# Kernel tuning notes

Hardware: AMD Instinct MI355X
Metric: run time of the kernel (lower is better)

Reference implementation:

```python
import jax, jax.numpy as jnp
import numpy as np

B, N, M = 4, 2048, 2048
QUERY_DIM = 512
CONTEXT_DIM = 512
HEADS = 8
DIM_HEAD = 64
INNER = HEADS * DIM_HEAD  # 512
SCALE = DIM_HEAD ** -0.5


def setup_inputs() -> dict:
    key = jax.random.key(0)
    ks = jax.random.split(key, 7)
    x = jax.random.normal(ks[0], (B, N, QUERY_DIM), dtype=jnp.float32)
    context = jax.random.normal(ks[1], (B, M, CONTEXT_DIM), dtype=jnp.float32)
    mask = jax.random.randint(ks[2], (B, M), 0, 2) > 0  # bool key mask
    # Kaiming-uniform-ish init scale, like nn.Linear defaults
    Wq = jax.random.uniform(ks[3], (QUERY_DIM, INNER), dtype=jnp.float32,
                            minval=-1, maxval=1) * (QUERY_DIM ** -0.5)
    Wkv = jax.random.uniform(ks[4], (CONTEXT_DIM, 2 * INNER), dtype=jnp.float32,
                             minval=-1, maxval=1) * (CONTEXT_DIM ** -0.5)
    Wo = jax.random.uniform(ks[5], (INNER, QUERY_DIM), dtype=jnp.float32,
                            minval=-1, maxval=1) * (INNER ** -0.5)
    bo = jax.random.uniform(ks[6], (QUERY_DIM,), dtype=jnp.float32,
                            minval=-1, maxval=1) * (INNER ** -0.5)
    return {"x": x, "context": context, "mask": mask,
            "Wq": Wq, "Wkv": Wkv, "Wo": Wo, "bo": bo}


def reference(x, context, mask, Wq, Wkv, Wo, bo):
    # projections (no bias for q/kv, bias for out — as in the torch module)
    q = x @ Wq                       # [b, n, inner]
    kv = context @ Wkv               # [b, m, 2*inner]
    k, v = jnp.split(kv, 2, axis=-1)
    # split heads: b n (h d) -> b h n d
    def split_heads(t):
        b, n, _ = t.shape
        return t.reshape(b, n, HEADS, DIM_HEAD).transpose(0, 2, 1, 3)
    q, k, v = split_heads(q), split_heads(k), split_heads(v)
    sim = jnp.einsum('bhid,bhjd->bhij', q, k) * SCALE  # [b, h, n, m]
    max_neg = -jnp.finfo(sim.dtype).max
    sim = jnp.where(mask[:, None, None, :], sim, max_neg)
    attn = jax.nn.softmax(sim, axis=-1)
    out = jnp.einsum('bhij,bhjd->bhid', attn, v)       # [b, h, n, d]
    out = out.transpose(0, 2, 1, 3).reshape(x.shape[0], x.shape[1], INNER)
    return out @ Wo + bo
```

## Files before the change

### kernel.cpp

```cpp
#include <hip/hip_runtime.h>
#include <hip/hip_bf16.h>
#include <cstddef>

typedef __attribute__((ext_vector_type(8))) short short8;
typedef __attribute__((ext_vector_type(4))) float f32x4;

__device__ inline unsigned short f2bf(float f) {
  unsigned int u = __float_as_uint(f);
  u += 0x7fffu + ((u >> 16) & 1u);
  return (unsigned short)(u >> 16);
}
__device__ inline unsigned int pkbf(float a, float b) {
  __hip_bfloat162 h = __float22bfloat162_rn(make_float2(a, b));
  union { __hip_bfloat162 h2; unsigned int u; } cv;
  cv.h2 = h;
  return cv.u;
}
__device__ inline float bf2f_lo(unsigned int u) {
  return __uint_as_float(u << 16);
}
__device__ inline float bf2f_hi(unsigned int u) {
  return __uint_as_float(u & 0xFFFF0000u);
}

__global__ __launch_bounds__(256) void prep_kernel(
    const float* __restrict__ Wq, const float* __restrict__ Wkv,
    const float* __restrict__ Wo, const int* __restrict__ mask,
    unsigned short* __restrict__ Wq_t, unsigned short* __restrict__ Wkv_t,
    unsigned short* __restrict__ Wo_t, unsigned int* __restrict__ pmask) {
  const int z = blockIdx.z;
  if (z == 3) {
    if (blockIdx.y != 0) return;
    int idx = blockIdx.x * 256 + threadIdx.x;
    int bb = idx >> 10, rem = idx & 1023;
    int g = rem >> 5, rem2 = rem & 31;
    int lqv = rem2 >> 3, e = rem2 & 7;
    int ct = e >> 1, half = e & 1;
    int key0 = g * 64 + half * 32 + lqv * 8 + 2 * ct;
    const int* mb = mask + bb * 2048;
    pmask[idx] = (mb[key0] ? 0xFFFFu : 0u) | (mb[key0 + 1] ? 0xFFFF0000u : 0u);
    return;
  }
  const float* src = (z == 0) ? Wq : (z == 1) ? Wkv : Wo;
  unsigned short* dst = (z == 0) ? Wq_t : (z == 1) ? Wkv_t : Wo_t;
  const int R = 512, C = (z == 1) ? 1024 : 512;
  if (blockIdx.x * 64 >= C) return;
  __shared__ float tile[64][65];
  int c0 = blockIdx.x * 64, r0 = blockIdx.y * 64;
  int tx = threadIdx.x & 63, ty = threadIdx.x >> 6;
  for (int i = ty; i < 64; i += 4)
    tile[i][tx] = src[(size_t)(r0 + i) * C + c0 + tx];
  __syncthreads();
  for (int i = ty; i < 64; i += 4)
    dst[(size_t)(c0 + i) * R + r0 + tx] = f2bf(tile[tx][i]);
}

__global__ __launch_bounds__(256) void proj_kernel(
    const float* __restrict__ x, const float* __restrict__ context,
    const unsigned short* __restrict__ Wq_t, const unsigned short* __restrict__ Wkv_t,
    unsigned short* __restrict__ qb, unsigned short* __restrict__ kb,
    unsigned short* __restrict__ vtb, float qscale) {
  __shared__ unsigned short As[128][72];
  __shared__ unsigned short Bs[128][72];
  const int bid = blockIdx.x;
  const bool isq = bid < 256;
  const int lid = isq ? bid : bid - 256;
  const float* Af = isq ? x : context;
  const unsigned short* Bt = isq ? Wq_t : Wkv_t;
  const int bn = (isq ? (lid & 3) : (lid & 7)) * 128;
  const int bm = (isq ? (lid >> 2) : (lid >> 3)) * 128;
  const int K = 512;
  const int tid = threadIdx.x;
  const int wave = tid >> 6, lane = tid & 63;
  const int wr = (wave >> 1) * 64, wc = (wave & 1) * 64;
  const int l15 = lane & 15, lq = lane >> 4;
  const int sr = tid >> 3, sc = (tid & 7) * 8;
  f32x4 acc[4][4] = {};

  for (int k0 = 0; k0 < K; k0 += 64) {
    __syncthreads();
#pragma unroll
    for (int p = 0; p < 4; ++p) {
      int r = sr + p * 32;
      const float4 f0 = *(const float4*)(Af + (size_t)(bm + r) * K + k0 + sc);
      const float4 f1 = *(const float4*)(Af + (size_t)(bm + r) * K + k0 + sc + 4);
      uint4 u;
      u.x = pkbf(f0.x, f0.y);
      u.y = pkbf(f0.z, f0.w);
      u.z = pkbf(f1.x, f1.y);
      u.w = pkbf(f1.z, f1.w);
      *(uint4*)(&As[r][sc]) = u;
      *(uint4*)(&Bs[r][sc]) = *(const uint4*)(Bt + (size_t)(bn + r) * K + k0 + sc);
    }
    __syncthreads();
#pragma unroll
    for (int kk = 0; kk < 2; ++kk) {
      short8 af[4], bfr[4];
#pragma unroll
      for (int mt = 0; mt < 4; ++mt)
        af[mt] = *(const short8*)(&As[wr + mt * 16 + l15][kk * 32 + lq * 8]);
#pragma unroll
      for (int nt = 0; nt < 4; ++nt)
        bfr[nt] = *(const short8*)(&Bs[wc + nt * 16 + l15][kk * 32 + lq * 8]);
#pragma unroll
      for (int mt = 0; mt < 4; ++mt)
#pragma unroll
        for (int nt = 0; nt < 4; ++nt)
          acc[mt][nt] = __builtin_amdgcn_mfma_f32_16x16x32_bf16(af[mt], bfr[nt], acc[mt][nt], 0, 0, 0);
    }
  }

#pragma unroll
  for (int mt = 0; mt < 4; ++mt)
#pragma unroll
    for (int nt = 0; nt < 4; ++nt) {
      int row0 = bm + wr + mt * 16 + lq * 4;
      int col = bn + wc + nt * 16 + l15;
      if (isq) {
#pragma unroll
        for (int j = 0; j < 4; ++j)
          qb[(size_t)(row0 + j) * 512 + col] = f2bf(acc[mt][nt][j] * qscale);
      } else if (col < 512) {
#pragma unroll
        for (int j = 0; j < 4; ++j)
          kb[(size_t)(row0 + j) * 512 + col] = f2bf(acc[mt][nt][j]);
      } else {
        int bb = row0 >> 11, m = row0 & 2047;
        int hd = col - 512;
        uint2 w;
        w.x = pkbf(acc[mt][nt][0], acc[mt][nt][1]);
        w.y = pkbf(acc[mt][nt][2], acc[mt][nt][3]);
        *(uint2*)(vtb + ((size_t)bb * 512 + hd) * 2048 + m) = w;
      }
    }
}

__global__ __launch_bounds__(256) void outproj_kernel(
    const unsigned short* __restrict__ poA, const unsigned short* __restrict__ poB,
    const float* __restrict__ ls, const unsigned short* __restrict__ Bt,
    float* __restrict__ C0, const float* __restrict__ bias) {
  __shared__ unsigned short As[64][72];
  __shared__ unsigned short Bs[128][72];
  const int bm = blockIdx.y * 64, bn = blockIdx.x * 128;
  const int K = 512, N = 512;
  const int tid = threadIdx.x;
  const int wave = tid >> 6, lane = tid & 63;
  const int wr = (wave >> 1) * 32, wc = (wave & 1) * 64;
  const int l15 = lane & 15, lq = lane >> 4;
  const int sr = tid >> 3, sc = (tid & 7) * 8;
  f32x4 acc[2][4] = {};

  for (int k0 = 0; k0 < K; k0 += 64) {
    const int h = k0 >> 6;
    __syncthreads();
#pragma unroll
    for (int p = 0; p < 2; ++p) {
      int row = bm + sr + p * 32;
      uint4 ua = *(const uint4*)(poA + (size_t)row * 512 + k0 + sc);
      uint4 ub = *(const uint4*)(poB + (size_t)row * 512 + k0 + sc);
      float l = ls[(size_t)h * 8192 + row] + ls[65536 + (size_t)h * 8192 + row];
      float rl = 1.0f / l;
      uint4 u;
      u.x = pkbf((bf2f_lo(ua.x) + bf2f_lo(ub.x)) * rl, (bf2f_hi(ua.x) + bf2f_hi(ub.x)) * rl);
      u.y = pkbf((bf2f_lo(ua.y) + bf2f_lo(ub.y)) * rl, (bf2f_hi(ua.y) + bf2f_hi(ub.y)) * rl);
      u.z = pkbf((bf2f_lo(ua.z) + bf2f_lo(ub.z)) * rl, (bf2f_hi(ua.z) + bf2f_hi(ub.z)) * rl);
      u.w = pkbf((bf2f_lo(ua.w) + bf2f_lo(ub.w)) * rl, (bf2f_hi(ua.w) + bf2f_hi(ub.w)) * rl);
      *(uint4*)(&As[sr + p * 32][sc]) = u;
    }
#pragma unroll
    for (int p = 0; p < 4; ++p)
      *(uint4*)(&Bs[sr + p * 32][sc]) = *(const uint4*)(Bt + (size_t)(bn + sr + p * 32) * K + k0 + sc);
    __syncthreads();
#pragma unroll
    for (int kk = 0; kk < 2; ++kk) {
      short8 af[2], bfr[4];
#pragma unroll
      for (int mt = 0; mt < 2; ++mt)
        af[mt] = *(const short8*)(&As[wr + mt * 16 + l15][kk * 32 + lq * 8]);
#pragma unroll
      for (int nt = 0; nt < 4; ++nt)
        bfr[nt] = *(const short8*)(&Bs[wc + nt * 16 + l15][kk * 32 + lq * 8]);
#pragma unroll
      for (int mt = 0; mt < 2; ++mt)
#pragma unroll
        for (int nt = 0; nt < 4; ++nt)
          acc[mt][nt] = __builtin_amdgcn_mfma_f32_16x16x32_bf16(af[mt], bfr[nt], acc[mt][nt], 0, 0, 0);
    }
  }

#pragma unroll
  for (int mt = 0; mt < 2; ++mt)
#pragma unroll
    for (int nt = 0; nt < 4; ++nt) {
      int row0 = bm + wr + mt * 16 + lq * 4;
      int col = bn + wc + nt * 16 + l15;
#pragma unroll
      for (int j = 0; j < 4; ++j)
        C0[(size_t)(row0 + j) * N + col] = acc[mt][nt][j] + bias[col];
    }
}

__global__ __launch_bounds__(256, 3) void attn_kernel(
    const unsigned short* __restrict__ Q, const unsigned short* __restrict__ Kb,
    const unsigned short* __restrict__ Vt, const unsigned int* __restrict__ pmask,
    unsigned short* __restrict__ poA, unsigned short* __restrict__ poB,
    float* __restrict__ ls) {
  __shared__ unsigned short Ks[2][64][72];
  __shared__ unsigned short Vs[2][64][72];
  const int b = blockIdx.x >> 3, h = blockIdx.x & 7;
  const int z = blockIdx.z;
  const int tid = threadIdx.x, lane = tid & 63;
  const int wave = tid >> 6;
  const int l15 = lane & 15, lq = lane >> 4;
  const int wrow = blockIdx.y * 128 + wave * 32;

  const unsigned short* Qr0 = Q + (size_t)(b * 2048 + wrow + l15) * 512 + h * 64;
  const unsigned short* Qr1 = Q + (size_t)(b * 2048 + wrow + 16 + l15) * 512 + h * 64;
  short8 q00 = *(const short8*)(Qr0 + lq * 8);
  short8 q01 = *(const short8*)(Qr0 + 32 + lq * 8);
  short8 q10 = *(const short8*)(Qr1 + lq * 8);
  short8 q11 = *(const short8*)(Qr1 + 32 + lq * 8);

  const short8 vones = {0x3F80, 0x3F80, 0x3F80, 0x3F80,
                        0x3F80, 0x3F80, 0x3F80, 0x3F80};

  f32x4 o0[4] = {}, o1[4] = {};
  f32x4 ol0 = {}, ol1 = {};

  const unsigned short* Kg = Kb + (size_t)b * 2048 * 512 + h * 64;
  const unsigned short* Vg = Vt + (size_t)(b * 8 + h) * 64 * 2048;
  const unsigned int* Pm = pmask + b * 1024;

  const int str = tid >> 3;
  const int stc = (tid & 7) * 8;
  const int kprow = ((str & 7) >> 1) * 16 + ((str >> 3) & 3) * 4 + (str & 1);

  const int mb0 = z << 10;

  uint4 krA0 = *(const uint4*)(Kg + (size_t)(mb0 + str) * 512 + stc);
  uint4 krA1 = *(const uint4*)(Kg + (size_t)(mb0 + str + 32) * 512 + stc);
  uint4 krB0 = *(const uint4*)(Kg + (size_t)(mb0 + 64 + str) * 512 + stc);
  uint4 krB1 = *(const uint4*)(Kg + (size_t)(mb0 + 64 + str + 32) * 512 + stc);
  uint4 vrA0 = *(const uint4*)(Vg + (size_t)str * 2048 + mb0 + stc);
  uint4 vrA1 = *(const uint4*)(Vg + (size_t)(str + 32) * 2048 + mb0 + stc);
  uint4 vrB0 = *(const uint4*)(Vg + (size_t)str * 2048 + mb0 + 64 + stc);
  uint4 vrB1 = *(const uint4*)(Vg + (size_t)(str + 32) * 2048 + mb0 + 64 + stc);

  for (int mb = mb0; mb < mb0 + 1024; mb += 128) {
    __syncthreads();
    *(uint4*)(&Ks[0][kprow][stc])     = krA0;
    *(uint4*)(&Ks[0][kprow + 2][stc]) = krA1;
    *(uint4*)(&Ks[1][kprow][stc])     = krB0;
    *(uint4*)(&Ks[1][kprow + 2][stc]) = krB1;
    *(uint4*)(&Vs[0][str][stc])       = vrA0;
    *(uint4*)(&Vs[0][str + 32][stc])  = vrA1;
    *(uint4*)(&Vs[1][str][stc])       = vrB0;
    *(uint4*)(&Vs[1][str + 32][stc])  = vrB1;
    __syncthreads();
    if (mb + 128 < mb0 + 1024) {
      const int nx = mb + 128;
      krA0 = *(const uint4*)(Kg + (size_t)(nx + str) * 512 + stc);
      krA1 = *(const uint4*)(Kg + (size_t)(nx + str + 32) * 512 + stc);
      krB0 = *(const uint4*)(Kg + (size_t)(nx + 64 + str) * 512 + stc);
      krB1 = *(const uint4*)(Kg + (size_t)(nx + 64 + str + 32) * 512 + stc);
      vrA0 = *(const uint4*)(Vg + (size_t)str * 2048 + nx + stc);
      vrA1 = *(const uint4*)(Vg + (size_t)(str + 32) * 2048 + nx + stc);
      vrB0 = *(const uint4*)(Vg + (size_t)str * 2048 + nx + 64 + stc);
      vrB1 = *(const uint4*)(Vg + (size_t)(str + 32) * 2048 + nx + 64 + stc);
    }

#pragma unroll
    for (int g = 0; g < 2; ++g) {
      const uint4 m0 = *(const uint4*)(Pm + ((mb >> 6) + g) * 32 + lq * 8);
      const uint4 m1 = *(const uint4*)(Pm + ((mb >> 6) + g) * 32 + lq * 8 + 4);

      f32x4 s0[4] = {}, s1[4] = {};
#pragma unroll
      for (int ct = 0; ct < 4; ++ct) {
        short8 kf = *(const short8*)(&Ks[g][ct * 16 + l15][lq * 8]);
        s0[ct] = __builtin_amdgcn_mfma_f32_16x16x32_bf16(kf, q00, s0[ct], 0, 0, 0);
        s1[ct] = __builtin_amdgcn_mfma_f32_16x16x32_bf16(kf, q10, s1[ct], 0, 0, 0);
      }
#pragma unroll
      for (int ct = 0; ct < 4; ++ct) {
        short8 kf = *(const short8*)(&Ks[g][ct * 16 + l15][32 + lq * 8]);
        s0[ct] = __builtin_amdgcn_mfma_f32_16x16x32_bf16(kf, q01, s0[ct], 0, 0, 0);
        s1[ct] = __builtin_amdgcn_mfma_f32_16x16x32_bf16(kf, q11, s1[ct], 0, 0, 0);
      }

      unsigned int xp0[4][2], xp1[4][2];
#pragma unroll
      for (int ct = 0; ct < 4; ++ct) {
        float a0 = __builtin_amdgcn_exp2f(s0[ct][0]);
        float a1 = __builtin_amdgcn_exp2f(s0[ct][1]);
        float a2 = __builtin_amdgcn_exp2f(s0[ct][2]);
        float a3 = __builtin_amdgcn_exp2f(s0[ct][3]);
        xp0[ct][0] = pkbf(a0, a1);
        xp0[ct][1] = pkbf(a2, a3);
        float c0 = __builtin_amdgcn_exp2f(s1[ct][0]);
        float c1 = __builtin_amdgcn_exp2f(s1[ct][1]);
        float c2 = __builtin_amdgcn_exp2f(s1[ct][2]);
        float c3 = __builtin_amdgcn_exp2f(s1[ct][3]);
        xp1[ct][0] = pkbf(c0, c1);
        xp1[ct][1] = pkbf(c2, c3);
      }

      xp0[0][0] &= m0.x; xp0[0][1] &= m0.y; xp0[1][0] &= m0.z; xp0[1][1] &= m0.w;
      xp0[2][0] &= m1.x; xp0[2][1] &= m1.y; xp0[3][0] &= m1.z; xp0[3][1] &= m1.w;
      xp1[0][0] &= m0.x; xp1[0][1] &= m0.y; xp1[1][0] &= m0.z; xp1[1][1] &= m0.w;
      xp1[2][0] &= m1.x; xp1[2][1] &= m1.y; xp1[3][0] &= m1.z; xp1[3][1] &= m1.w;

#pragma unroll
      for (int kk = 0; kk < 2; ++kk) {
        union { unsigned int u[4]; short8 s8; } pc0, pc1;
        pc0.u[0] = xp0[0][kk]; pc0.u[1] = xp0[1][kk];
        pc0.u[2] = xp0[2][kk]; pc0.u[3] = xp0[3][kk];
        pc1.u[0] = xp1[0][kk]; pc1.u[1] = xp1[1][kk];
        pc1.u[2] = xp1[2][kk]; pc1.u[3] = xp1[3][kk];
#pragma unroll
        for (int dt = 0; dt < 4; ++dt) {
          short8 vf = *(const short8*)(&Vs[g][dt * 16 + l15][kk * 32 + lq * 8]);
          o0[dt] = __builtin_amdgcn_mfma_f32_16x16x32_bf16(vf, pc0.s8, o0[dt], 0, 0, 0);
          o1[dt] = __builtin_amdgcn_mfma_f32_16x16x32_bf16(vf, pc1.s8, o1[dt], 0, 0, 0);
        }
        ol0 = __builtin_amdgcn_mfma_f32_16x16x32_bf16(vones, pc0.s8, ol0, 0, 0, 0);
        ol1 = __builtin_amdgcn_mfma_f32_16x16x32_bf16(vones, pc1.s8, ol1, 0, 0, 0);
      }
    }
  }

  unsigned short* po = z ? poB : poA;
  unsigned short* Or0 = po + (size_t)(b * 2048 + wrow + l15) * 512 + h * 64;
  unsigned short* Or1 = po + (size_t)(b * 2048 + wrow + 16 + l15) * 512 + h * 64;
#pragma unroll
  for (int dt = 0; dt < 4; ++dt) {
    *(unsigned int*)(Or0 + dt * 16 + lq * 4)     = pkbf(o0[dt][0], o0[dt][1]);
    *(unsigned int*)(Or0 + dt * 16 + lq * 4 + 2) = pkbf(o0[dt][2], o0[dt][3]);
    *(unsigned int*)(Or1 + dt * 16 + lq * 4)     = pkbf(o1[dt][0], o1[dt][1]);
    *(unsigned int*)(Or1 + dt * 16 + lq * 4 + 2) = pkbf(o1[dt][2], o1[dt][3]);
  }
  if (lq == 0) {
    ls[((size_t)z * 8 + h) * 8192 + b * 2048 + wrow + l15]      = ol0[0];
    ls[((size_t)z * 8 + h) * 8192 + b * 2048 + wrow + 16 + l15] = ol1[0];
  }
}

extern "C" void kernel_launch(void* const* d_in, const int* in_sizes, int n_in,
                              void* d_out, int out_size, void* d_ws, size_t ws_size,
                              hipStream_t stream) {
  const float* x       = (const float*)d_in[0];
  const float* context = (const float*)d_in[1];
  const int*   mask    = (const int*)d_in[2];
  const float* Wq      = (const float*)d_in[3];
  const float* Wkv     = (const float*)d_in[4];
  const float* Wo      = (const float*)d_in[5];
  const float* bo      = (const float*)d_in[6];
  float* out = (float*)d_out;

  char* ws = (char*)d_ws;
  unsigned short* Wq_t  = (unsigned short*)(ws + 0);
  unsigned short* Wkv_t = (unsigned short*)(ws + 524288);
  unsigned short* Wo_t  = (unsigned short*)(ws + 1572864);
  unsigned short* qb    = (unsigned short*)(ws + 2097152);
  unsigned short* kb    = (unsigned short*)(ws + 10485760);
  unsigned short* vtb   = (unsigned short*)(ws + 18874368);
  unsigned short* poA   = (unsigned short*)(ws + 27262976);
  unsigned short* poB   = (unsigned short*)(ws + 35651584);
  unsigned int* pmask   = (unsigned int*)(ws + 44040192);
  float* ls             = (float*)(ws + 44056576);

  const float QSCALE = 0.125f * 1.44269504088896f;

  prep_kernel<<<dim3(16, 8, 4), 256, 0, stream>>>(Wq, Wkv, Wo, mask,
                                                  Wq_t, Wkv_t, Wo_t, pmask);
  proj_kernel<<<dim3(768), 256, 0, stream>>>(x, context, Wq_t, Wkv_t,
                                             qb, kb, vtb, QSCALE);
  attn_kernel<<<dim3(32, 16, 2), 256, 0, stream>>>(qb, kb, vtb, pmask,
                                                   poA, poB, ls);
  outproj_kernel<<<dim3(4, 128), 256, 0, stream>>>(poA, poB, ls, Wo_t, out, bo);
}
```

Baseline: 108.4 us.

## Prefetch next K tile into registers in projection GEMM and precompute reciprocals

The projection GEMM now loads the next K-slice of A (fp32) and B (bf16) into registers while the MFMA loop works on the current shared-memory tile. This hides global-load latency behind compute, and launch bounds now ask for 3 blocks per CU. In the output projection, the per-row softmax normaliser reciprocals for all heads are computed once into shared memory instead of re-reading ls and dividing on each K step. The prefetch raises register pressure, which the occupancy hint may force into spills.

Result: faster. 104.3 us, median of 2 (-3.8%).

```diff
diff --git a/kernel.cpp b/kernel.cpp
--- a/kernel.cpp
+++ b/kernel.cpp
@@ -55,7 +55,7 @@
     dst[(size_t)(c0 + i) * R + r0 + tx] = f2bf(tile[tx][i]);
 }
 
-__global__ __launch_bounds__(256) void proj_kernel(
+__global__ __launch_bounds__(256, 3) void proj_kernel(
     const float* __restrict__ x, const float* __restrict__ context,
     const unsigned short* __restrict__ Wq_t, const unsigned short* __restrict__ Wkv_t,
     unsigned short* __restrict__ qb, unsigned short* __restrict__ kb,
@@ -77,22 +77,54 @@
   const int sr = tid >> 3, sc = (tid & 7) * 8;
   f32x4 acc[4][4] = {};
 
+  float4 fA0a = *(const float4*)(Af + (size_t)(bm + sr) * K + sc);
+  float4 fA0b = *(const float4*)(Af + (size_t)(bm + sr) * K + sc + 4);
+  float4 fA1a = *(const float4*)(Af + (size_t)(bm + sr + 32) * K + sc);
+  float4 fA1b = *(const float4*)(Af + (size_t)(bm + sr + 32) * K + sc + 4);
+  float4 fA2a = *(const float4*)(Af + (size_t)(bm + sr + 64) * K + sc);
+  float4 fA2b = *(const float4*)(Af + (size_t)(bm + sr + 64) * K + sc + 4);
+  float4 fA3a = *(const float4*)(Af + (size_t)(bm + sr + 96) * K + sc);
+  float4 fA3b = *(const float4*)(Af + (size_t)(bm + sr + 96) * K + sc + 4);
+  uint4 uB0 = *(const uint4*)(Bt + (size_t)(bn + sr) * K + sc);
+  uint4 uB1 = *(const uint4*)(Bt + (size_t)(bn + sr + 32) * K + sc);
+  uint4 uB2 = *(const uint4*)(Bt + (size_t)(bn + sr + 64) * K + sc);
+  uint4 uB3 = *(const uint4*)(Bt + (size_t)(bn + sr + 96) * K + sc);
+
   for (int k0 = 0; k0 < K; k0 += 64) {
     __syncthreads();
-#pragma unroll
-    for (int p = 0; p < 4; ++p) {
-      int r = sr + p * 32;
-      const float4 f0 = *(const float4*)(Af + (size_t)(bm + r) * K + k0 + sc);
-      const float4 f1 = *(const float4*)(Af + (size_t)(bm + r) * K + k0 + sc + 4);
-      uint4 u;
-      u.x = pkbf(f0.x, f0.y);
-      u.y = pkbf(f0.z, f0.w);
-      u.z = pkbf(f1.x, f1.y);
-      u.w = pkbf(f1.z, f1.w);
-      *(uint4*)(&As[r][sc]) = u;
-      *(uint4*)(&Bs[r][sc]) = *(const uint4*)(Bt + (size_t)(bn + r) * K + k0 + sc);
-    }
-    __syncthreads();
+    uint4 u;
+    u.x = pkbf(fA0a.x, fA0a.y); u.y = pkbf(fA0a.z, fA0a.w);
+    u.z = pkbf(fA0b.x, fA0b.y); u.w = pkbf(fA0b.z, fA0b.w);
+    *(uint4*)(&As[sr][sc]) = u;
+    u.x = pkbf(fA1a.x, fA1a.y); u.y = pkbf(fA1a.z, fA1a.w);
+    u.z = pkbf(fA1b.x, fA1b.y); u.w = pkbf(fA1b.z, fA1b.w);
+    *(uint4*)(&As[sr + 32][sc]) = u;
+    u.x = pkbf(fA2a.x, fA2a.y); u.y = pkbf(fA2a.z, fA2a.w);
+    u.z = pkbf(fA2b.x, fA2b.y); u.w = pkbf(fA2b.z, fA2b.w);
+    *(uint4*)(&As[sr + 64][sc]) = u;
+    u.x = pkbf(fA3a.x, fA3a.y); u.y = pkbf(fA3a.z, fA3a.w);
+    u.z = pkbf(fA3b.x, fA3b.y); u.w = pkbf(fA3b.z, fA3b.w);
+    *(uint4*)(&As[sr + 96][sc]) = u;
+    *(uint4*)(&Bs[sr][sc])      = uB0;
+    *(uint4*)(&Bs[sr + 32][sc]) = uB1;
+    *(uint4*)(&Bs[sr + 64][sc]) = uB2;
+    *(uint4*)(&Bs[sr + 96][sc]) = uB3;
+    __syncthreads();
+    if (k0 + 64 < K) {
+      const int kn = k0 + 64;
+      fA0a = *(const float4*)(Af + (size_t)(bm + sr) * K + kn + sc);
+      fA0b = *(const float4*)(Af + (size_t)(bm + sr) * K + kn + sc + 4);
+      fA1a = *(const float4*)(Af + (size_t)(bm + sr + 32) * K + kn + sc);
+      fA1b = *(const float4*)(Af + (size_t)(bm + sr + 32) * K + kn + sc + 4);
+      fA2a = *(const float4*)(Af + (size_t)(bm + sr + 64) * K + kn + sc);
+      fA2b = *(const float4*)(Af + (size_t)(bm + sr + 64) * K + kn + sc + 4);
+      fA3a = *(const float4*)(Af + (size_t)(bm + sr + 96) * K + kn + sc);
+      fA3b = *(const float4*)(Af + (size_t)(bm + sr + 96) * K + kn + sc + 4);
+      uB0 = *(const uint4*)(Bt + (size_t)(bn + sr) * K + kn + sc);
+      uB1 = *(const uint4*)(Bt + (size_t)(bn + sr + 32) * K + kn + sc);
+      uB2 = *(const uint4*)(Bt + (size_t)(bn + sr + 64) * K + kn + sc);
+      uB3 = *(const uint4*)(Bt + (size_t)(bn + sr + 96) * K + kn + sc);
+    }
 #pragma unroll
     for (int kk = 0; kk < 2; ++kk) {
       short8 af[4], bfr[4];
@@ -141,6 +173,7 @@
     float* __restrict__ C0, const float* __restrict__ bias) {
   __shared__ unsigned short As[64][72];
   __shared__ unsigned short Bs[128][72];
+  __shared__ float rls[512];
   const int bm = blockIdx.y * 64, bn = blockIdx.x * 128;
   const int K = 512, N = 512;
   const int tid = threadIdx.x;
@@ -150,6 +183,13 @@
   const int sr = tid >> 3, sc = (tid & 7) * 8;
   f32x4 acc[2][4] = {};
 
+#pragma unroll
+  for (int it = 0; it < 2; ++it) {
+    int idx = tid + it * 256;
+    int hh = idx >> 6, row = bm + (idx & 63);
+    rls[idx] = 1.0f / (ls[(size_t)hh * 8192 + row] + ls[65536 + (size_t)hh * 8192 + row]);
+  }
+
   for (int k0 = 0; k0 < K; k0 += 64) {
     const int h = k0 >> 6;
     __syncthreads();
@@ -158,8 +198,7 @@
       int row = bm + sr + p * 32;
       uint4 ua = *(const uint4*)(poA + (size_t)row * 512 + k0 + sc);
       uint4 ub = *(const uint4*)(poB + (size_t)row * 512 + k0 + sc);
-      float l = ls[(size_t)h * 8192 + row] + ls[65536 + (size_t)h * 8192 + row];
-      float rl = 1.0f / l;
+      float rl = rls[h * 64 + sr + p * 32];
       uint4 u;
       u.x = pkbf((bf2f_lo(ua.x) + bf2f_lo(ub.x)) * rl, (bf2f_hi(ua.x) + bf2f_hi(ub.x)) * rl);
       u.y = pkbf((bf2f_lo(ua.y) + bf2f_lo(ub.y)) * rl, (bf2f_hi(ua.y) + bf2f_hi(ub.y)) * rl);
```
